# Kernel optimization log

Measured on AMD Instinct MI355X. Metric: run time of the kernel, lower is better.

Reference implementation:

```python
import jax, jax.numpy as jnp
import numpy as np

B, T, C, H = 8, 1024, 768, 12
D = C // H


def setup_inputs() -> dict:
    key = jax.random.key(0)
    ks = jax.random.split(key, 12)
    s = lambda fan_in: 1.0 / np.sqrt(fan_in)
    return {
        "x": jax.random.normal(ks[0], (B, T, C), dtype=jnp.float32),
        "ln_w": jnp.ones((C,), jnp.float32),
        "ln_b": jnp.zeros((C,), jnp.float32),
        "w_qkv": jax.random.normal(ks[1], (C, 3 * C), jnp.float32) * s(C),
        "b_qkv": jax.random.normal(ks[2], (3 * C,), jnp.float32) * 0.02,
        "w_out": jax.random.normal(ks[3], (C, C), jnp.float32) * s(C),
        "b_out": jax.random.normal(ks[4], (C,), jnp.float32) * 0.02,
        "w_c1": jax.random.normal(ks[5], (C, 4 * C), jnp.float32) * s(C),
        "b_c1": jax.random.normal(ks[6], (4 * C,), jnp.float32) * 0.02,
        "w_c2": jax.random.normal(ks[7], (4 * C, C), jnp.float32) * s(4 * C),
        "b_c2": jax.random.normal(ks[8], (C,), jnp.float32) * 0.02,
    }


def _layer_norm(x, w, b, eps=1e-5):
    mu = jnp.mean(x, axis=-1, keepdims=True)
    var = jnp.var(x, axis=-1, keepdims=True)
    return (x - mu) * jax.lax.rsqrt(var + eps) * w + b


def reference(x, ln_w, ln_b, w_qkv, b_qkv, w_out, b_out, w_c1, b_c1, w_c2, b_c2):
    b, t, c = x.shape
    # NOTE: both norms in Block share the SAME params (source re-assigns self.layer_norm)
    h = _layer_norm(x, ln_w, ln_b)
    qkv = h @ w_qkv + b_qkv  # [b,t,3c]
    # source splits as (k, q, v) in that order
    k, q, v = jnp.split(qkv, 3, axis=-1)
    k = k.reshape(b, t, H, D).transpose(0, 2, 1, 3)  # [b,h,t,d]
    q = q.reshape(b, t, H, D).transpose(0, 2, 1, 3)
    v = v.reshape(b, t, H, D).transpose(0, 2, 1, 3)
    # NOTE: no 1/sqrt(d) scaling in the source
    scores = jnp.einsum("bhqd,bhkd->bhqk", q, k)
    mask = jnp.tril(jnp.ones((t, t), dtype=bool))
    scores = jnp.where(mask, scores, -jnp.inf)
    attn = jax.nn.softmax(scores, axis=-1)
    y = jnp.einsum("bhqk,bhkd->bhqd", attn, v)
    y = y.transpose(0, 2, 1, 3).reshape(b, t, c)
    y = y @ w_out + b_out
    x = x + y
    h = _layer_norm(x, ln_w, ln_b)
    m = jax.nn.gelu(h @ w_c1 + b_c1, approximate=False) @ w_c2 + b_c2
    return x + m
```

## Files before the change

kernel.cpp:

```cpp
#include <hip/hip_runtime.h>
#include <hip/hip_bf16.h>
#include <math.h>

typedef short v4s __attribute__((ext_vector_type(4)));
typedef short v8s __attribute__((ext_vector_type(8)));
typedef float v4f __attribute__((ext_vector_type(4)));
typedef unsigned short us8 __attribute__((ext_vector_type(8)));

#if __has_builtin(__builtin_amdgcn_mfma_f32_16x16x16bf16_1k)
#define MFMA16(a, b, c) __builtin_amdgcn_mfma_f32_16x16x16bf16_1k(a, b, c, 0, 0, 0)
#else
__device__ inline v4f mfma16_fb(v4s a, v4s b, v4f c) {
    v8s a8 = {a[0], a[1], a[2], a[3], 0, 0, 0, 0};
    v8s b8 = {b[0], b[1], b[2], b[3], 0, 0, 0, 0};
    return __builtin_amdgcn_mfma_f32_16x16x32_bf16(a8, b8, c, 0, 0, 0);
}
#define MFMA16(a, b, c) mfma16_fb(a, b, c)
#endif

#define MFMA32(a, b, c) __builtin_amdgcn_mfma_f32_16x16x32_bf16(a, b, c, 0, 0, 0)

__device__ inline unsigned short f2bf(float f) {
    __hip_bfloat16 h = __float2bfloat16(f);
    union { __hip_bfloat16 h; unsigned short u; } cv;
    cv.h = h;
    return cv.u;
}

__device__ inline void gld16(const void* g, void* l) {
    __builtin_amdgcn_global_load_lds((const __attribute__((address_space(1))) void*)g,
                                     (__attribute__((address_space(3))) void*)l, 16, 0, 0);
}

__device__ inline float gelu_fast(float v) {
    const float z2 = 1.5957691216057308f * (v + 0.044715f * v * v * v);
    return v / (1.0f + __expf(-z2));
}

__global__ __launch_bounds__(256) void transpose_cvt(const float* __restrict__ in,
                                                     unsigned short* __restrict__ out,
                                                     int R, int Cn) {
    __shared__ float t[32][33];
    const int tid = threadIdx.x;
    const int tx = tid & 31, ty = tid >> 5;
    const int bx = blockIdx.x, by = blockIdx.y;
#pragma unroll
    for (int i = 0; i < 4; ++i) {
        int r = by * 32 + ty + i * 8;
        int c = bx * 32 + tx;
        t[ty + i * 8][tx] = in[(size_t)r * Cn + c];
    }
    __syncthreads();
#pragma unroll
    for (int i = 0; i < 4; ++i) {
        out[(size_t)(bx * 32 + ty + i * 8) * R + by * 32 + tx] = f2bf(t[tx][ty + i * 8]);
    }
}

__global__ __launch_bounds__(256) void ln_row(const float* __restrict__ x,
                                              const float* __restrict__ lw,
                                              const float* __restrict__ lb,
                                              unsigned short* __restrict__ out) {
    const int row = blockIdx.x;
    const int tid = threadIdx.x;
    const float* xr = x + (size_t)row * 768;
    float v0 = xr[tid], v1 = xr[tid + 256], v2 = xr[tid + 512];
    float s = v0 + v1 + v2;
    float q = v0 * v0 + v1 * v1 + v2 * v2;
#pragma unroll
    for (int o = 1; o < 64; o <<= 1) {
        s += __shfl_xor(s, o);
        q += __shfl_xor(q, o);
    }
    __shared__ float rs[4], rq[4];
    const int w = tid >> 6;
    if ((tid & 63) == 0) { rs[w] = s; rq[w] = q; }
    __syncthreads();
    s = rs[0] + rs[1] + rs[2] + rs[3];
    q = rq[0] + rq[1] + rq[2] + rq[3];
    const float mean = s * (1.0f / 768.0f);
    const float var = q * (1.0f / 768.0f) - mean * mean;
    const float rstd = rsqrtf(var + 1e-5f);
    unsigned short* orow = out + (size_t)row * 768;
    orow[tid] = f2bf((v0 - mean) * rstd * lw[tid] + lb[tid]);
    orow[tid + 256] = f2bf((v1 - mean) * rstd * lw[tid + 256] + lb[tid + 256]);
    orow[tid + 512] = f2bf((v2 - mean) * rstd * lw[tid + 512] + lb[tid + 512]);
}

template <int EPI>
__global__ __launch_bounds__(256) void gemm_bf16(const unsigned short* __restrict__ A,
                                                 const unsigned short* __restrict__ BT,
                                                 const float* __restrict__ bias,
                                                 const float* __restrict__ resid,
                                                 void* __restrict__ outp,
                                                 int M, int N, int K) {
    __shared__ __align__(16) unsigned short As[128 * 64];
    __shared__ __align__(16) unsigned short Bs[128 * 64];
    const int tid = threadIdx.x;
    const int lane = tid & 63;
    const int w = tid >> 6;
    const int g = lane >> 4;
    const int c16 = lane & 15;
    const int row0 = blockIdx.x * 128;
    const int col0 = blockIdx.y * 128;
    const int wm = w & 1, wn = w >> 1;

    v4f acc[4][4];
#pragma unroll
    for (int m = 0; m < 4; ++m)
#pragma unroll
        for (int n = 0; n < 4; ++n) acc[m][n] = (v4f){0.f, 0.f, 0.f, 0.f};

    const unsigned short* ap[4];
    const unsigned short* bp[4];
#pragma unroll
    for (int i = 0; i < 4; ++i) {
        const int c = (i * 4 + w) * 64 + lane;
        const int r = c >> 3;
        const int dc = (c & 7) ^ (r & 7);
        ap[i] = A + (size_t)(row0 + r) * K + dc * 8;
        bp[i] = BT + (size_t)(col0 + r) * K + dc * 8;
    }

    const int nk = K >> 6;
    for (int kt = 0; kt < nk; ++kt) {
        __syncthreads();
#pragma unroll
        for (int i = 0; i < 4; ++i) {
            const int c = (i * 4 + w) * 64 + lane;
            gld16(ap[i], As + (size_t)c * 8);
            gld16(bp[i], Bs + (size_t)c * 8);
            ap[i] += 64;
            bp[i] += 64;
        }
        __syncthreads();
#pragma unroll
        for (int ks = 0; ks < 2; ++ks) {
            const int koff = ks * 64 + 16 * g;
            v8s af[4], bf[4];
#pragma unroll
            for (int m = 0; m < 4; ++m) {
                const int r = wm * 64 + m * 16 + c16;
                af[m] = *(const v8s*)((const char*)As + r * 128 + (koff ^ ((r & 7) << 4)));
            }
#pragma unroll
            for (int n = 0; n < 4; ++n) {
                const int r = wn * 64 + n * 16 + c16;
                bf[n] = *(const v8s*)((const char*)Bs + r * 128 + (koff ^ ((r & 7) << 4)));
            }
#pragma unroll
            for (int m = 0; m < 4; ++m)
#pragma unroll
                for (int n = 0; n < 4; ++n) acc[m][n] = MFMA32(af[m], bf[n], acc[m][n]);
        }
    }
#pragma unroll
    for (int m = 0; m < 4; ++m)
#pragma unroll
        for (int n = 0; n < 4; ++n)
#pragma unroll
            for (int r = 0; r < 4; ++r) {
                const int row = row0 + wm * 64 + m * 16 + 4 * g + r;
                const int col = col0 + wn * 64 + n * 16 + c16;
                float v = acc[m][n][r] + bias[col];
                if (EPI == 1) v += resid[(size_t)row * N + col];
                if (EPI == 2) v = gelu_fast(v);
                if (EPI == 1)
                    ((float*)outp)[(size_t)row * N + col] = v;
                else
                    ((unsigned short*)outp)[(size_t)row * N + col] = f2bf(v);
            }
}

__device__ inline void attn_tile(const unsigned short* Ks, const unsigned short* Vt,
                                 unsigned short* Psw, const v8s* qf8, v4f* yacc,
                                 float& mrun, float& lrun, bool diag, int mask0,
                                 int g, int c16) {
    v4f st[4];
#pragma unroll
    for (int kb = 0; kb < 4; ++kb) st[kb] = (v4f){0.f, 0.f, 0.f, 0.f};
#pragma unroll
    for (int ks = 0; ks < 2; ++ks) {
        const int koff = ks * 64 + 16 * g;
#pragma unroll
        for (int kb = 0; kb < 4; ++kb) {
            const int r = kb * 16 + c16;
            const v8s kf = *(const v8s*)((const char*)Ks + r * 128 + (koff ^ ((r & 7) << 4)));
            st[kb] = MFMA32(kf, qf8[ks], st[kb]);
        }
    }

    float pmax = -__builtin_inff();
    if (diag) {
#pragma unroll
        for (int kb = 0; kb < 4; ++kb)
#pragma unroll
            for (int r = 0; r < 4; ++r) {
                if (kb * 16 + 4 * g + r > mask0) st[kb][r] = -__builtin_inff();
                pmax = fmaxf(pmax, st[kb][r]);
            }
    } else {
#pragma unroll
        for (int kb = 0; kb < 4; ++kb)
#pragma unroll
            for (int r = 0; r < 4; ++r) pmax = fmaxf(pmax, st[kb][r]);
    }
    pmax = fmaxf(pmax, __shfl_xor(pmax, 16));
    pmax = fmaxf(pmax, __shfl_xor(pmax, 32));
    const float mnew = fmaxf(mrun, pmax);
    const float scale = __expf(mrun - mnew);
    float psum = 0.0f;
#pragma unroll
    for (int kb = 0; kb < 4; ++kb) {
        v4s pw;
#pragma unroll
        for (int r = 0; r < 4; ++r) {
            const float pv = __expf(st[kb][r] - mnew);
            psum += pv;
            pw[r] = (short)f2bf(pv);
        }
        *(v4s*)((char*)Psw + c16 * 136 + kb * 32 + 8 * g) = pw;
    }
    psum += __shfl_xor(psum, 16);
    psum += __shfl_xor(psum, 32);
    lrun = lrun * scale + psum;
    mrun = mnew;

    float scr[4];
#pragma unroll
    for (int r = 0; r < 4; ++r) scr[r] = __shfl(scale, g * 4 + r);
#pragma unroll
    for (int d = 0; d < 4; ++d)
#pragma unroll
        for (int r = 0; r < 4; ++r) yacc[d][r] *= scr[r];

#pragma unroll
    for (int ks = 0; ks < 4; ++ks) {
        const v4s pf = *(const v4s*)((const char*)Psw + c16 * 136 + ks * 32 + 8 * g);
#pragma unroll
        for (int d = 0; d < 4; ++d) {
            const v4s vf = *(const v4s*)((const char*)Vt + (d * 16 + c16) * 136 + ks * 32 + 8 * g);
            yacc[d] = MFMA16(pf, vf, yacc[d]);
        }
    }
}

__global__ __launch_bounds__(256) void attn_kernel(const unsigned short* __restrict__ qkv,
                                                   unsigned short* __restrict__ y) {
    __shared__ __align__(16) unsigned short Ks[64 * 64];
    __shared__ __align__(16) unsigned short Vt[64 * 68];
    __shared__ __align__(16) unsigned short Ps[4][16 * 68];
    const int tid = threadIdx.x;
    const int lane = tid & 63;
    const int w = tid >> 6;
    const int g = lane >> 4;
    const int c16 = lane & 15;
    const int p = blockIdx.x;
    const int h = blockIdx.y, b = blockIdx.z;
    const int qtA = 15 - p, qtB = p;
    const int tokA = b * 1024 + qtA * 64;
    const int tokB = b * 1024 + qtB * 64;

    v8s qfA[2], qfB[2];
    {
        const unsigned short* qbA = qkv + (size_t)(tokA + w * 16 + c16) * 2304 + 768 + h * 64;
        const unsigned short* qbB = qkv + (size_t)(tokB + w * 16 + c16) * 2304 + 768 + h * 64;
#pragma unroll
        for (int ks = 0; ks < 2; ++ks) {
            qfA[ks] = *(const v8s*)(qbA + ks * 32 + 8 * g);
            qfB[ks] = *(const v8s*)(qbB + ks * 32 + 8 * g);
        }
    }

    v4f yA[4], yB[4];
#pragma unroll
    for (int d = 0; d < 4; ++d) {
        yA[d] = (v4f){0.f, 0.f, 0.f, 0.f};
        yB[d] = (v4f){0.f, 0.f, 0.f, 0.f};
    }
    float mA = -__builtin_inff(), lA = 0.0f;
    float mB = -__builtin_inff(), lB = 0.0f;
    const int qrow = w * 16 + c16;

    for (int kt = 0; kt <= qtA; ++kt) {
        const int tokk = b * 1024 + kt * 64;
        __syncthreads();
#pragma unroll
        for (int i = 0; i < 2; ++i) {
            const int c = (i * 4 + w) * 64 + lane;
            const int kk = c >> 3;
            const int dc = (c & 7) ^ (kk & 7);
            gld16(qkv + (size_t)(tokk + kk) * 2304 + h * 64 + dc * 8, Ks + (size_t)c * 8);
        }
#pragma unroll
        for (int it = 0; it < 2; ++it) {
            const int off = (it * 256 + tid) * 8;
            const int kk = off >> 6, d0 = off & 63;
            us8 vv = *(const us8*)(qkv + (size_t)(tokk + kk) * 2304 + 1536 + h * 64 + d0);
#pragma unroll
            for (int j = 0; j < 8; ++j) Vt[(d0 + j) * 68 + kk] = vv[j];
        }
        __syncthreads();

        attn_tile(Ks, Vt, &Ps[w][0], qfA, yA, mA, lA, kt == qtA, qrow, g, c16);
        if (kt <= qtB)
            attn_tile(Ks, Vt, &Ps[w][0], qfB, yB, mB, lB, kt == qtB, qrow, g, c16);
    }

    {
        const float inv = 1.0f / lA;
        float invr[4];
#pragma unroll
        for (int r = 0; r < 4; ++r) invr[r] = __shfl(inv, g * 4 + r);
#pragma unroll
        for (int d = 0; d < 4; ++d)
#pragma unroll
            for (int r = 0; r < 4; ++r) {
                const int row = tokA + w * 16 + 4 * g + r;
                const int col = h * 64 + d * 16 + c16;
                y[(size_t)row * 768 + col] = f2bf(yA[d][r] * invr[r]);
            }
    }
    {
        const float inv = 1.0f / lB;
        float invr[4];
#pragma unroll
        for (int r = 0; r < 4; ++r) invr[r] = __shfl(inv, g * 4 + r);
#pragma unroll
        for (int d = 0; d < 4; ++d)
#pragma unroll
            for (int r = 0; r < 4; ++r) {
                const int row = tokB + w * 16 + 4 * g + r;
                const int col = h * 64 + d * 16 + c16;
                y[(size_t)row * 768 + col] = f2bf(yB[d][r] * invr[r]);
            }
    }
}

extern "C" void kernel_launch(void* const* d_in, const int* in_sizes, int n_in,
                              void* d_out, int out_size, void* d_ws, size_t ws_size,
                              hipStream_t stream) {
    const float* x = (const float*)d_in[0];
    const float* ln_w = (const float*)d_in[1];
    const float* ln_b = (const float*)d_in[2];
    const float* w_qkv = (const float*)d_in[3];
    const float* b_qkv = (const float*)d_in[4];
    const float* w_out = (const float*)d_in[5];
    const float* b_out = (const float*)d_in[6];
    const float* w_c1 = (const float*)d_in[7];
    const float* b_c1 = (const float*)d_in[8];
    const float* w_c2 = (const float*)d_in[9];
    const float* b_c2 = (const float*)d_in[10];
    float* out = (float*)d_out;

    char* ws = (char*)d_ws;
    unsigned short* wTqkv = (unsigned short*)(ws + 0);
    unsigned short* wTout = (unsigned short*)(ws + 3538944);
    unsigned short* wTc1 = (unsigned short*)(ws + 4718592);
    unsigned short* wTc2 = (unsigned short*)(ws + 9437184);
    unsigned short* hbuf = (unsigned short*)(ws + 14155776);
    unsigned short* qkvb = (unsigned short*)(ws + 26738688);
    unsigned short* ybuf = (unsigned short*)(ws + 64487424);
    float* x2 = (float*)(ws + 77070336);
    unsigned short* m1 = qkvb;

    transpose_cvt<<<dim3(2304 / 32, 768 / 32), 256, 0, stream>>>(w_qkv, wTqkv, 768, 2304);
    transpose_cvt<<<dim3(768 / 32, 768 / 32), 256, 0, stream>>>(w_out, wTout, 768, 768);
    transpose_cvt<<<dim3(3072 / 32, 768 / 32), 256, 0, stream>>>(w_c1, wTc1, 768, 3072);
    transpose_cvt<<<dim3(768 / 32, 3072 / 32), 256, 0, stream>>>(w_c2, wTc2, 3072, 768);

    ln_row<<<8192, 256, 0, stream>>>(x, ln_w, ln_b, hbuf);
    gemm_bf16<0><<<dim3(64, 18), 256, 0, stream>>>(hbuf, wTqkv, b_qkv, nullptr, qkvb, 8192, 2304, 768);
    attn_kernel<<<dim3(8, 12, 8), 256, 0, stream>>>(qkvb, ybuf);
    gemm_bf16<1><<<dim3(64, 6), 256, 0, stream>>>(ybuf, wTout, b_out, x, x2, 8192, 768, 768);
    ln_row<<<8192, 256, 0, stream>>>(x2, ln_w, ln_b, hbuf);
    gemm_bf16<2><<<dim3(64, 24), 256, 0, stream>>>(hbuf, wTc1, b_c1, nullptr, m1, 8192, 3072, 768);
    gemm_bf16<1><<<dim3(64, 6), 256, 0, stream>>>(m1, wTc2, b_c2, x2, out, 8192, 768, 3072);
}
```

Before: 367.1 us.

## Keep softmax probabilities in registers, skip masked diagonal blocks, lazy rescale

The probability tile is fed to the PV MFMA straight from registers, because the S-transposed accumulator layout already matches the A-operand layout. This removes the LDS write and read round-trip and the per-wave P buffer. On diagonal tiles, key blocks that lie wholly above the causal boundary for a wave are skipped in both the QK and PV MFMA loops. The running-max rescale of the accumulator is now done only when the new max exceeds the old one by more than a threshold, which saves exp and multiply work but lets unnormalized values grow up to e^8.

```diff
diff --git a/kernel.cpp b/kernel.cpp
--- a/kernel.cpp
+++ b/kernel.cpp
@@ -173,9 +173,9 @@
 }
 
 __device__ inline void attn_tile(const unsigned short* Ks, const unsigned short* Vt,
-                                 unsigned short* Psw, const v8s* qf8, v4f* yacc,
-                                 float& mrun, float& lrun, bool diag, int mask0,
-                                 int g, int c16) {
+                                 const v8s* qf8, v4f* yacc,
+                                 float& mrun, float& lrun, bool diag, int qrow,
+                                 int w, int g, int c16) {
     v4f st[4];
 #pragma unroll
     for (int kb = 0; kb < 4; ++kb) st[kb] = (v4f){0.f, 0.f, 0.f, 0.f};
@@ -184,6 +184,7 @@
         const int koff = ks * 64 + 16 * g;
 #pragma unroll
         for (int kb = 0; kb < 4; ++kb) {
+            if (diag && kb > w) continue;
             const int r = kb * 16 + c16;
             const v8s kf = *(const v8s*)((const char*)Ks + r * 128 + (koff ^ ((r & 7) << 4)));
             st[kb] = MFMA32(kf, qf8[ks], st[kb]);
@@ -196,7 +197,7 @@
         for (int kb = 0; kb < 4; ++kb)
 #pragma unroll
             for (int r = 0; r < 4; ++r) {
-                if (kb * 16 + 4 * g + r > mask0) st[kb][r] = -__builtin_inff();
+                if (kb > w || kb * 16 + 4 * g + r > qrow) st[kb][r] = -__builtin_inff();
                 pmax = fmaxf(pmax, st[kb][r]);
             }
     } else {
@@ -207,40 +208,42 @@
     }
     pmax = fmaxf(pmax, __shfl_xor(pmax, 16));
     pmax = fmaxf(pmax, __shfl_xor(pmax, 32));
-    const float mnew = fmaxf(mrun, pmax);
-    const float scale = __expf(mrun - mnew);
+
+    if (!__all(pmax <= mrun + 8.0f)) {
+        const float mnew = fmaxf(mrun, pmax);
+        const float scale = __expf(mrun - mnew);
+        lrun *= scale;
+        float scr[4];
+#pragma unroll
+        for (int r = 0; r < 4; ++r) scr[r] = __shfl(scale, g * 4 + r);
+#pragma unroll
+        for (int d = 0; d < 4; ++d)
+#pragma unroll
+            for (int r = 0; r < 4; ++r) yacc[d][r] *= scr[r];
+        mrun = mnew;
+    }
+
     float psum = 0.0f;
-#pragma unroll
-    for (int kb = 0; kb < 4; ++kb) {
-        v4s pw;
+    v4s pw[4];
+#pragma unroll
+    for (int kb = 0; kb < 4; ++kb)
 #pragma unroll
         for (int r = 0; r < 4; ++r) {
-            const float pv = __expf(st[kb][r] - mnew);
+            const float pv = __expf(st[kb][r] - mrun);
             psum += pv;
-            pw[r] = (short)f2bf(pv);
-        }
-        *(v4s*)((char*)Psw + c16 * 136 + kb * 32 + 8 * g) = pw;
-    }
+            pw[kb][r] = (short)f2bf(pv);
+        }
     psum += __shfl_xor(psum, 16);
     psum += __shfl_xor(psum, 32);
-    lrun = lrun * scale + psum;
-    mrun = mnew;
-
-    float scr[4];
-#pragma unroll
-    for (int r = 0; r < 4; ++r) scr[r] = __shfl(scale, g * 4 + r);
-#pragma unroll
-    for (int d = 0; d < 4; ++d)
-#pragma unroll
-        for (int r = 0; r < 4; ++r) yacc[d][r] *= scr[r];
+    lrun += psum;
 
 #pragma unroll
     for (int ks = 0; ks < 4; ++ks) {
-        const v4s pf = *(const v4s*)((const char*)Psw + c16 * 136 + ks * 32 + 8 * g);
+        if (diag && ks > w) continue;
 #pragma unroll
         for (int d = 0; d < 4; ++d) {
             const v4s vf = *(const v4s*)((const char*)Vt + (d * 16 + c16) * 136 + ks * 32 + 8 * g);
-            yacc[d] = MFMA16(pf, vf, yacc[d]);
+            yacc[d] = MFMA16(pw[ks], vf, yacc[d]);
         }
     }
 }
@@ -249,7 +252,6 @@
                                                    unsigned short* __restrict__ y) {
     __shared__ __align__(16) unsigned short Ks[64 * 64];
     __shared__ __align__(16) unsigned short Vt[64 * 68];
-    __shared__ __align__(16) unsigned short Ps[4][16 * 68];
     const int tid = threadIdx.x;
     const int lane = tid & 63;
     const int w = tid >> 6;
@@ -302,9 +304,9 @@
         }
         __syncthreads();
 
-        attn_tile(Ks, Vt, &Ps[w][0], qfA, yA, mA, lA, kt == qtA, qrow, g, c16);
+        attn_tile(Ks, Vt, qfA, yA, mA, lA, kt == qtA, qrow, w, g, c16);
         if (kt <= qtB)
-            attn_tile(Ks, Vt, &Ps[w][0], qfB, yB, mB, lB, kt == qtB, qrow, g, c16);
+            attn_tile(Ks, Vt, qfB, yB, mB, lB, kt == qtB, qrow, w, g, c16);
     }
 
     {
```

New measurement: 351.1 us. -4.3%, faster.
